# Performance work log

Hardware: AMD Instinct MI355X
Metric: run time of the kernel (lower is better)

## Reference

```python
import jax, jax.numpy as jnp
import numpy as np

D_MODEL = 1024
D_INNER = 2048
D_STATE = 16
DT_RANK = 64
D_CONV = 4
EPS = 1e-5
B_SZ, L = 2, 2048


def setup_inputs() -> dict:
    key = jax.random.key(0)
    ks = jax.random.split(key, 8)
    s = 0.02
    inp = {
        "x": jax.random.normal(ks[0], (B_SZ, L, D_MODEL), jnp.float32),
        "in_proj_w": jax.random.normal(ks[1], (D_MODEL, 2 * D_INNER), jnp.float32) * s,
        "conv_w": jax.random.normal(ks[2], (D_INNER, 1, D_CONV), jnp.float32) * s,
        "conv_b": jnp.zeros((D_INNER,), jnp.float32),
        "x_proj_w": jax.random.normal(ks[3], (D_INNER, DT_RANK + 2 * D_STATE), jnp.float32) * s,
        "dt_proj_w": jax.random.normal(ks[4], (DT_RANK, D_INNER), jnp.float32) * s,
        "dt_proj_b": jax.random.normal(ks[5], (D_INNER,), jnp.float32) * s,
        "A_log": jnp.log(jnp.broadcast_to(jnp.arange(1, D_STATE + 1, dtype=jnp.float32), (D_INNER, D_STATE))),
        "D": jnp.ones((D_INNER,), jnp.float32),
        "out_proj_w": jax.random.normal(ks[6], (D_INNER, D_MODEL), jnp.float32) * s,
        "norm_w": jnp.ones((D_MODEL,), jnp.float32),
    }
    return inp


def _silu(x):
    return x * jax.nn.sigmoid(x)


def reference(x, in_proj_w, conv_w, conv_b, x_proj_w, dt_proj_w, dt_proj_b,
              A_log, D, out_proj_w, norm_w):
    b, l, d = x.shape
    # RMSNorm
    xn = x * jax.lax.rsqrt(jnp.mean(x * x, axis=-1, keepdims=True) + EPS) * norm_w
    # in_proj -> split into x branch and residual (gate) branch
    x_and_res = xn @ in_proj_w                      # (b, l, 2*d_inner)
    xi, res = jnp.split(x_and_res, 2, axis=-1)
    # causal depthwise conv1d (pad left d_conv-1, equivalent to torch pad+truncate)
    xc = jax.lax.conv_general_dilated(
        xi.transpose(0, 2, 1),                      # (b, d_inner, l)
        conv_w,                                     # (d_inner, 1, d_conv) = OIH
        window_strides=(1,),
        padding=[(D_CONV - 1, 0)],
        feature_group_count=D_INNER,
        dimension_numbers=("NCH", "OIH", "NCH"),
    ) + conv_b[None, :, None]
    xi = _silu(xc.transpose(0, 2, 1))               # (b, l, d_inner)
    # SSM parameters
    x_dbl = xi @ x_proj_w                           # (b, l, dt_rank + 2n)
    delta, Bm, Cm = jnp.split(x_dbl, [DT_RANK, DT_RANK + D_STATE], axis=-1)
    delta = jax.nn.softplus(delta @ dt_proj_w + dt_proj_b)   # (b, l, d_inner)
    A = -jnp.exp(A_log)                             # (d_inner, n)
    # discretize
    deltaA = jnp.exp(delta[..., None] * A)                          # (b,l,d,n)
    deltaB_u = delta[..., None] * Bm[:, :, None, :] * xi[..., None]  # (b,l,d,n)
    # selective scan over sequence length via lax.scan
    def step(state, inputs):
        dA_t, dBu_t, C_t = inputs                   # (b,d,n),(b,d,n),(b,n)
        state = dA_t * state + dBu_t
        y_t = jnp.einsum("bdn,bn->bd", state, C_t)
        return state, y_t
    state0 = jnp.zeros((b, D_INNER, D_STATE), xi.dtype)
    _, ys = jax.lax.scan(
        step, state0,
        (deltaA.transpose(1, 0, 2, 3), deltaB_u.transpose(1, 0, 2, 3), Cm.transpose(1, 0, 2)),
    )                                               # ys: (l, b, d_inner)
    y = ys.transpose(1, 0, 2) + xi * D              # skip connection D*u
    y = y * _silu(res)                              # gate
    out = y @ out_proj_w + x                        # out_proj + residual add
    return out
```

## Files before the change

### kernel.cpp

```cpp
#include <hip/hip_runtime.h>
#include <cstdint>

#define D_MODEL 1024
#define D_INNER 2048
#define NSTATE  16
#define DT_RANK 64
#define SEQ     2048
#define NBATCH  2
#define NTOK    (NBATCH * SEQ)

#define NC      32
#define CHK     64
#define NGRP    8

typedef float  f32x4  __attribute__((ext_vector_type(4)));
typedef __bf16 bf16x8 __attribute__((ext_vector_type(8)));
typedef short  s16x8  __attribute__((ext_vector_type(8)));

__device__ __forceinline__ unsigned short f2bf(float f) {
  union { float f; uint32_t u; } a; a.f = f;
  uint32_t u = a.u;
  uint32_t r = (u + 0x7FFFu + ((u >> 16) & 1u)) >> 16;
  return (unsigned short)r;
}
__device__ __forceinline__ float bf2f(unsigned short h) {
  union { uint32_t u; float f; } a; a.u = ((uint32_t)h) << 16;
  return a.f;
}

__device__ __forceinline__ void gload16(const void* g, void* l) {
  __builtin_amdgcn_global_load_lds((__attribute__((address_space(1))) void*)g,
                                   (__attribute__((address_space(3))) void*)l,
                                   16, 0, 0);
}

__device__ __forceinline__ void rms_body(const float* __restrict__ x, const float* __restrict__ nw,
                                         unsigned short* __restrict__ xn, int row, float* red) {
  const float4 v = ((const float4*)(x + (size_t)row * D_MODEL))[threadIdx.x];
  float ss = v.x*v.x + v.y*v.y + v.z*v.z + v.w*v.w;
  #pragma unroll
  for (int m = 32; m; m >>= 1) ss += __shfl_xor(ss, m);
  if ((threadIdx.x & 63) == 0) red[threadIdx.x >> 6] = ss;
  __syncthreads();
  const float tot = red[0] + red[1] + red[2] + red[3];
  const float rs = rsqrtf(tot * (1.0f / D_MODEL) + 1e-5f);
  const float4 w = ((const float4*)nw)[threadIdx.x];
  ushort4 o;
  o.x = f2bf(v.x * rs * w.x);
  o.y = f2bf(v.y * rs * w.y);
  o.z = f2bf(v.z * rs * w.z);
  o.w = f2bf(v.w * rs * w.w);
  ((ushort4*)(xn + (size_t)row * D_MODEL))[threadIdx.x] = o;
}

__device__ __forceinline__ void tr_body(const float* __restrict__ W, unsigned short* __restrict__ Wt,
                                        int K, int N, int Npad, int bx, int by, float (*tile)[33]) {
  const int tx = threadIdx.x & 31, ty = threadIdx.x >> 5;
  const int kt = by * 32, nt = bx * 32;
  #pragma unroll
  for (int i = 0; i < 4; ++i) {
    const int k = kt + ty + i*8, n = nt + tx;
    tile[ty + i*8][tx] = (k < K && n < N) ? W[(size_t)k * N + n] : 0.0f;
  }
  __syncthreads();
  #pragma unroll
  for (int i = 0; i < 4; ++i) {
    const int n = nt + ty + i*8, k = kt + tx;
    if (n < Npad && k < K) Wt[(size_t)n * K + k] = f2bf(tile[tx][ty + i*8]);
  }
}

__global__ __launch_bounds__(256) void prep_fused_kernel(const float* x, const float* nw, unsigned short* xn,
                                                         const float* W1, unsigned short* W1t,
                                                         const float* W2, unsigned short* W2t,
                                                         const float* W3, unsigned short* W3t,
                                                         const float* W4, unsigned short* W4t) {
  __shared__ float shbuf[32][33];
  const int b = blockIdx.x;
  if (b < 4096) {
    rms_body(x, nw, xn, b, &shbuf[0][0]);
  } else if (b < 8192) {
    const int i = b - 4096;
    tr_body(W1, W1t, 1024, 4096, 4096, i & 127, i >> 7, shbuf);
  } else if (b < 8448) {
    const int i = b - 8192;
    tr_body(W2, W2t, 2048, 96, 128, i & 3, i >> 2, shbuf);
  } else if (b < 8576) {
    const int i = b - 8448;
    tr_body(W3, W3t, 64, 2048, 2048, i & 63, i >> 6, shbuf);
  } else {
    const int i = b - 8576;
    tr_body(W4, W4t, 2048, 1024, 1024, i & 31, i >> 5, shbuf);
  }
}

template<int MODE>
__device__ __forceinline__ void gemm_body(const unsigned short* __restrict__ A,
                                          const unsigned short* __restrict__ Bt,
                                          const int M, const int N, const int K,
                                          void* __restrict__ out0,
                                          void* __restrict__ out1,
                                          const float* __restrict__ extra) {
  __shared__ __align__(16) unsigned short sA[2][128 * 32];
  __shared__ __align__(16) unsigned short sB[2][128 * 32];
  const int tid = threadIdx.x;
  const int w = tid >> 6, lane = tid & 63;
  const int m0 = blockIdx.y * 128, n0 = blockIdx.x * 128;
  const int wm = w >> 1, wn = w & 1;
  const int lr = lane & 15, kq = lane >> 4;

  f32x4 acc[4][4] = {};

  const int r0 = tid >> 2;
  const int qb = ((tid & 3) ^ (r0 & 3)) * 16;
  const char* pA0 = (const char*)A + ((size_t)(m0 + r0)      * K) * 2 + qb;
  const char* pA1 = (const char*)A + ((size_t)(m0 + r0 + 64) * K) * 2 + qb;
  const char* pB0 = (const char*)Bt + ((size_t)(n0 + r0)      * K) * 2 + qb;
  const char* pB1 = (const char*)Bt + ((size_t)(n0 + r0 + 64) * K) * 2 + qb;

  const int kqs = (kq ^ (lr & 3)) * 8;

  auto stage = [&](int p, int k0) {
    gload16(pA0 + (size_t)k0 * 2, (char*)sA[p] + w * 1024);
    gload16(pA1 + (size_t)k0 * 2, (char*)sA[p] + 4096 + w * 1024);
    gload16(pB0 + (size_t)k0 * 2, (char*)sB[p] + w * 1024);
    gload16(pB1 + (size_t)k0 * 2, (char*)sB[p] + 4096 + w * 1024);
  };
  auto compute = [&](int p) {
    const unsigned short* pa = sA[p] + (wm*64 + lr) * 32 + kqs;
    const unsigned short* pb = sB[p] + (wn*64 + lr) * 32 + kqs;
    bf16x8 af[4], bb[4];
    #pragma unroll
    for (int mf = 0; mf < 4; ++mf)
      af[mf] = __builtin_bit_cast(bf16x8, *(const s16x8*)(pa + mf * 16 * 32));
    #pragma unroll
    for (int nf = 0; nf < 4; ++nf)
      bb[nf] = __builtin_bit_cast(bf16x8, *(const s16x8*)(pb + nf * 16 * 32));
    #pragma unroll
    for (int mf = 0; mf < 4; ++mf)
      #pragma unroll
      for (int nf = 0; nf < 4; ++nf)
        acc[mf][nf] = __builtin_amdgcn_mfma_f32_16x16x32_bf16(af[mf], bb[nf], acc[mf][nf], 0, 0, 0);
  };

  stage(0, 0);
  __syncthreads();
  int p = 0;
  for (int k0 = 32; k0 < K; k0 += 32) {
    stage(p ^ 1, k0);
    compute(p);
    __syncthreads();
    p ^= 1;
  }
  compute(p);

  #pragma unroll
  for (int mf = 0; mf < 4; ++mf) {
    #pragma unroll
    for (int nf = 0; nf < 4; ++nf) {
      #pragma unroll
      for (int r = 0; r < 4; ++r) {
        const int row = m0 + wm*64 + mf*16 + kq*4 + r;
        const int col = n0 + wn*64 + nf*16 + lr;
        const float v = acc[mf][nf][r];
        if constexpr (MODE == 0) {
          if (col < D_INNER) ((unsigned short*)out0)[(size_t)row * D_INNER + col] = f2bf(v);
          else               ((unsigned short*)out1)[(size_t)row * D_INNER + (col - D_INNER)] = f2bf(v);
        } else if constexpr (MODE == 1) {
          if (col < DT_RANK) ((unsigned short*)out0)[(size_t)row * DT_RANK + col] = f2bf(v);
          else if (col < DT_RANK + 2*NSTATE) ((float*)out1)[(size_t)row * (2*NSTATE) + (col - DT_RANK)] = v;
        } else if constexpr (MODE == 2) {
          const float t = v + extra[col];
          const float sp = (t > 30.0f) ? t : __logf(1.0f + __expf(t));
          ((unsigned short*)out0)[(size_t)row * D_INNER + col] = f2bf(sp);
        } else {
          ((float*)out0)[(size_t)row * D_MODEL + col] = v + extra[(size_t)row * D_MODEL + col];
        }
      }
    }
  }
}

__global__ __launch_bounds__(256) void g0_inproj_kernel(const unsigned short* A, const unsigned short* Bt,
                                                        int M, int N, int K, void* o0, void* o1, const float* ex) {
  gemm_body<0>(A, Bt, M, N, K, o0, o1, ex);
}
__global__ __launch_bounds__(256) void g1_xproj_kernel(const unsigned short* A, const unsigned short* Bt,
                                                       int M, int N, int K, void* o0, void* o1, const float* ex) {
  gemm_body<1>(A, Bt, M, N, K, o0, o1, ex);
}
__global__ __launch_bounds__(256) void g2_dtproj_kernel(const unsigned short* A, const unsigned short* Bt,
                                                        int M, int N, int K, void* o0, void* o1, const float* ex) {
  gemm_body<2>(A, Bt, M, N, K, o0, o1, ex);
}
__global__ __launch_bounds__(256) void g3_outproj_kernel(const unsigned short* A, const unsigned short* Bt,
                                                         int M, int N, int K, void* o0, void* o1, const float* ex) {
  gemm_body<3>(A, Bt, M, N, K, o0, o1, ex);
}

__global__ __launch_bounds__(256) void conv_silu_kernel(const unsigned short* __restrict__ xi_raw,
                                                        const float* __restrict__ cw,
                                                        const float* __restrict__ cb,
                                                        unsigned short* __restrict__ xi) {
  const int t = blockIdx.x * 256 + threadIdx.x;
  const int d8 = (t & 255) * 8;
  const int row = t >> 8;
  const int l = row & (SEQ - 1);

  float acc[8];
  #pragma unroll
  for (int c = 0; c < 8; c += 4) {
    const f32x4 bv = *(const f32x4*)(cb + d8 + c);
    acc[c+0] = bv[0]; acc[c+1] = bv[1]; acc[c+2] = bv[2]; acc[c+3] = bv[3];
  }
  f32x4 wv[8];
  #pragma unroll
  for (int c = 0; c < 8; ++c) wv[c] = ((const f32x4*)cw)[d8 + c];

  #pragma unroll
  for (int tap = 0; tap < 4; ++tap) {
    const int lp = l - 3 + tap;
    if (lp >= 0) {
      const s16x8 v = *(const s16x8*)(xi_raw + (size_t)(row - 3 + tap) * D_INNER + d8);
      #pragma unroll
      for (int c = 0; c < 8; ++c)
        acc[c] += wv[c][tap] * bf2f((unsigned short)v[c]);
    }
  }
  s16x8 o;
  #pragma unroll
  for (int c = 0; c < 8; ++c) {
    const float a = acc[c] / (1.0f + __expf(-acc[c]));
    o[c] = (short)f2bf(a);
  }
  *(s16x8*)(xi + (size_t)row * D_INNER + d8) = o;
}

template<int PASS>
__global__ __launch_bounds__(256) void scan_pass_kernel(const unsigned short* __restrict__ delta,
                                                        const unsigned short* __restrict__ xi,
                                                        const unsigned short* __restrict__ res,
                                                        const float* __restrict__ BC,
                                                        const float* __restrict__ A_log,
                                                        const float* __restrict__ Dv,
                                                        const float* __restrict__ initS,
                                                        float* __restrict__ aprodOut,
                                                        float* __restrict__ sendOut,
                                                        unsigned short* __restrict__ yg) {
  const int tid = threadIdx.x;
  const int db = blockIdx.x & 7;
  const int c  = (blockIdx.x >> 3) & (NC - 1);
  const int b  = blockIdx.x >> 8;
  const int d  = db * 256 + tid;
  const int row0 = b * SEQ + c * CHK;
  const size_t ob = ((size_t)(b * NC + c) * D_INNER + d) * 16;

  float Ac[16];
  #pragma unroll
  for (int q = 0; q < 4; ++q) {
    f32x4 t = ((const f32x4*)(A_log + (size_t)d * 16))[q];
    Ac[q*4+0] = -expf(t[0]); Ac[q*4+1] = -expf(t[1]);
    Ac[q*4+2] = -expf(t[2]); Ac[q*4+3] = -expf(t[3]);
  }
  float s[16];
  float ap[16];
  if constexpr (PASS == 0) {
    #pragma unroll
    for (int n = 0; n < 16; ++n) { s[n] = 0.0f; ap[n] = 1.0f; }
  } else {
    #pragma unroll
    for (int q = 0; q < 4; ++q)
      ((f32x4*)s)[q] = ((const f32x4*)(initS + ob))[q];
  }
  float Dd = 0.0f;
  if constexpr (PASS == 1) Dd = Dv[d];

  __shared__ float bcbuf[2][8][32];
  auto stageg = [&](int g, int p) {
    bcbuf[p][tid >> 5][tid & 31] = BC[(size_t)(row0 + g * 8) * 32 + tid];
  };
  stageg(0, 0);

  for (int g = 0; g < NGRP; ++g) {
    unsigned short dl[8], uu[8], rr[8];
    #pragma unroll
    for (int j = 0; j < 8; ++j) {
      const size_t row = (size_t)(row0 + g * 8 + j) * D_INNER + d;
      dl[j] = delta[row];
      uu[j] = xi[row];
      if constexpr (PASS == 1) rr[j] = res[row];
    }
    __syncthreads();
    if (g + 1 < NGRP) stageg(g + 1, (g + 1) & 1);

    #pragma unroll
    for (int j = 0; j < 8; ++j) {
      const float dlt = bf2f(dl[j]);
      const float u   = bf2f(uu[j]);
      const float dlu = dlt * u;
      float bc[32];
      #pragma unroll
      for (int q = 0; q < (PASS ? 8 : 4); ++q)
        ((f32x4*)bc)[q] = ((const f32x4*)(&bcbuf[g & 1][j][0]))[q];
      #pragma unroll
      for (int n = 0; n < 16; ++n) {
        const float dA = __expf(dlt * Ac[n]);
        s[n] = dA * s[n] + dlu * bc[n];
        if constexpr (PASS == 0) ap[n] *= dA;
      }
      if constexpr (PASS == 1) {
        float y = 0.0f;
        #pragma unroll
        for (int n = 0; n < 16; ++n) y += s[n] * bc[16 + n];
        const float r = bf2f(rr[j]);
        const float o = (y + u * Dd) * (r / (1.0f + __expf(-r)));
        yg[(size_t)(row0 + g * 8 + j) * D_INNER + d] = f2bf(o);
      }
    }
  }

  if constexpr (PASS == 0) {
    #pragma unroll
    for (int q = 0; q < 4; ++q) {
      ((f32x4*)(aprodOut + ob))[q] = ((f32x4*)ap)[q];
      ((f32x4*)(sendOut + ob))[q]  = ((f32x4*)s)[q];
    }
  }
}

__global__ __launch_bounds__(256) void scan_combine_kernel(const float* __restrict__ aprod,
                                                           const float* __restrict__ send,
                                                           float* __restrict__ initS) {
  const int t = blockIdx.x * 256 + threadIdx.x;
  const int b = t >> 13;
  const int rq = t & 8191;
  f32x4 carry = {0.0f, 0.0f, 0.0f, 0.0f};
  #pragma unroll
  for (int c = 0; c < NC; ++c) {
    const size_t idx = (size_t)(b * NC + c) * 8192 + rq;
    ((f32x4*)initS)[idx] = carry;
    const f32x4 a = ((const f32x4*)aprod)[idx];
    const f32x4 e = ((const f32x4*)send)[idx];
    carry = a * carry + e;
  }
}

extern "C" void kernel_launch(void* const* d_in, const int* in_sizes, int n_in,
                              void* d_out, int out_size, void* d_ws, size_t ws_size,
                              hipStream_t stream) {
  const float* x        = (const float*)d_in[0];
  const float* in_proj  = (const float*)d_in[1];
  const float* conv_w   = (const float*)d_in[2];
  const float* conv_b   = (const float*)d_in[3];
  const float* x_proj   = (const float*)d_in[4];
  const float* dt_proj  = (const float*)d_in[5];
  const float* dt_b     = (const float*)d_in[6];
  const float* A_log    = (const float*)d_in[7];
  const float* Dv       = (const float*)d_in[8];
  const float* out_proj = (const float*)d_in[9];
  const float* norm_w   = (const float*)d_in[10];

  char* ws = (char*)d_ws;
  size_t off = 0;
  auto alloc = [&](size_t bytes) {
    char* p = ws + off; off += (bytes + 255) & ~(size_t)255; return p;
  };
  unsigned short* xn     = (unsigned short*)alloc((size_t)NTOK * D_MODEL * 2);
  unsigned short* W1t    = (unsigned short*)alloc((size_t)(2 * D_INNER) * D_MODEL * 2);
  unsigned short* xi_raw = (unsigned short*)alloc((size_t)NTOK * D_INNER * 2);
  unsigned short* resb   = (unsigned short*)alloc((size_t)NTOK * D_INNER * 2);
  unsigned short* xi     = (unsigned short*)alloc((size_t)NTOK * D_INNER * 2);
  unsigned short* W2t    = (unsigned short*)alloc((size_t)128 * D_INNER * 2);
  unsigned short* dr     = (unsigned short*)alloc((size_t)NTOK * DT_RANK * 2);
  float*          BC     = (float*)alloc((size_t)NTOK * 32 * 4);
  unsigned short* W3t    = (unsigned short*)alloc((size_t)D_INNER * DT_RANK * 2);
  unsigned short* dlt    = (unsigned short*)alloc((size_t)NTOK * D_INNER * 2);
  unsigned short* ygb    = (unsigned short*)alloc((size_t)NTOK * D_INNER * 2);
  unsigned short* W4t    = (unsigned short*)alloc((size_t)D_MODEL * D_INNER * 2);

  float* aprod = (float*)xi_raw;
  float* send  = (float*)((char*)xi_raw + 8388608);
  float* initS = (float*)xn;

  prep_fused_kernel<<<10624, 256, 0, stream>>>(x, norm_w, xn,
                                               in_proj, W1t, x_proj, W2t,
                                               dt_proj, W3t, out_proj, W4t);

  g0_inproj_kernel<<<dim3(4096/128, 4096/128), 256, 0, stream>>>(xn, W1t, NTOK, 4096, 1024, xi_raw, resb, nullptr);
  conv_silu_kernel<<<NTOK, 256, 0, stream>>>(xi_raw, conv_w, conv_b, xi);
  g1_xproj_kernel<<<dim3(1, 4096/128), 256, 0, stream>>>(xi, W2t, NTOK, 128, 2048, dr, BC, nullptr);
  g2_dtproj_kernel<<<dim3(2048/128, 4096/128), 256, 0, stream>>>(dr, W3t, NTOK, 2048, 64, dlt, nullptr, dt_b);

  scan_pass_kernel<0><<<NBATCH * NC * (D_INNER/256), 256, 0, stream>>>(
      dlt, xi, nullptr, BC, A_log, nullptr, nullptr, aprod, send, nullptr);
  scan_combine_kernel<<<64, 256, 0, stream>>>(aprod, send, initS);
  scan_pass_kernel<1><<<NBATCH * NC * (D_INNER/256), 256, 0, stream>>>(
      dlt, xi, resb, BC, A_log, Dv, initS, nullptr, nullptr, ygb);

  g3_outproj_kernel<<<dim3(1024/128, 4096/128), 256, 0, stream>>>(ygb, W4t, NTOK, 1024, 2048, d_out, nullptr, x);
}
```

Before: 369.1 us.

## Give in_proj GEMM a dedicated 256x256 tile kernel with swizzled LDS

Swaps the generic 128x128 bf16 GEMM for in_proj with a dedicated kernel that uses 256x256 output tiles, 512 threads, BK=64, XOR-swizzled shared memory and direct global-to-LDS loads. Loads for the next K tile are interleaved with MFMA sub-steps, and s_setprio raises priority around the MFMA bursts. The goal is more operand reuse per tile and less LDS bank conflict and stall time on the largest GEMM. In exchange it uses 128KB of LDS per block and many accumulator registers, and the grid drops to 256 blocks, which may limit occupancy across the CUs.

New measurement: 350.3 us. -5.1%, faster.

```diff
diff --git a/kernel.cpp b/kernel.cpp
--- a/kernel.cpp
+++ b/kernel.cpp
@@ -94,6 +94,97 @@
   }
 }
 
+__global__ __launch_bounds__(512, 2) void g0_inproj_kernel(const unsigned short* __restrict__ A,
+                                                           const unsigned short* __restrict__ Bt,
+                                                           unsigned short* __restrict__ xiOut,
+                                                           unsigned short* __restrict__ resOut) {
+  constexpr int K  = 1024;
+  constexpr int NT = K / 64;
+  __shared__ __align__(16) unsigned short sA[2][256 * 64];
+  __shared__ __align__(16) unsigned short sB[2][256 * 64];
+  const int tid = threadIdx.x;
+  const int wid = tid >> 6, lane = tid & 63;
+  const int wm = wid >> 2, wn = wid & 3;
+  const int lr = lane & 15, kq = lane >> 4;
+  const int m0 = blockIdx.y * 256, n0 = blockIdx.x * 256;
+
+  f32x4 acc[8][4] = {};
+
+  const int srow = tid >> 3;
+  const int scol = 8 * ((tid & 7) ^ ((tid >> 3) & 7));
+  const unsigned short* gA = A  + (size_t)(m0 + srow) * K + scol;
+  const unsigned short* gB = Bt + (size_t)(n0 + srow) * K + scol;
+
+  const int xsw = (lr & 7) << 4;
+  const int cofs0 = ((kq * 16) ^ xsw) >> 1;
+  const int cofs1 = ((64 + kq * 16) ^ xsw) >> 1;
+  const int aRow = (wm * 128 + lr) * 64;
+  const int bRow = (wn * 64 + lr) * 64;
+
+  auto stage2 = [&](int p, int kt, int q) {
+    const int k0 = kt * 64;
+    gload16(gA + (size_t)q * 64 * K + k0, (char*)sA[p] + q * 8192 + tid * 16);
+    gload16(gB + (size_t)q * 64 * K + k0, (char*)sB[p] + q * 8192 + tid * 16);
+  };
+
+  #pragma unroll
+  for (int q = 0; q < 4; ++q) stage2(0, 0, q);
+  __syncthreads();
+
+  int p = 0;
+  for (int kt = 0; kt < NT; ++kt) {
+    const unsigned short* SA = sA[p];
+    const unsigned short* SB = sB[p];
+    bf16x8 b[4][2];
+    #pragma unroll
+    for (int q = 0; q < 4; ++q) {
+      bf16x8 a[2][2];
+      #pragma unroll
+      for (int mi = 0; mi < 2; ++mi) {
+        a[mi][0] = __builtin_bit_cast(bf16x8, *(const s16x8*)(SA + aRow + (2*q + mi) * 1024 + cofs0));
+        a[mi][1] = __builtin_bit_cast(bf16x8, *(const s16x8*)(SA + aRow + (2*q + mi) * 1024 + cofs1));
+      }
+      if (q == 0) {
+        #pragma unroll
+        for (int nf = 0; nf < 4; ++nf) {
+          b[nf][0] = __builtin_bit_cast(bf16x8, *(const s16x8*)(SB + bRow + nf * 1024 + cofs0));
+          b[nf][1] = __builtin_bit_cast(bf16x8, *(const s16x8*)(SB + bRow + nf * 1024 + cofs1));
+        }
+      }
+      if (kt + 1 < NT) stage2(p ^ 1, kt + 1, q);
+      __builtin_amdgcn_s_barrier();
+      __builtin_amdgcn_s_setprio(1);
+      #pragma unroll
+      for (int ks = 0; ks < 2; ++ks)
+        #pragma unroll
+        for (int mi = 0; mi < 2; ++mi)
+          #pragma unroll
+          for (int nf = 0; nf < 4; ++nf)
+            acc[2*q + mi][nf] = __builtin_amdgcn_mfma_f32_16x16x32_bf16(a[mi][ks], b[nf][ks], acc[2*q + mi][nf], 0, 0, 0);
+      __builtin_amdgcn_s_setprio(0);
+      __builtin_amdgcn_s_barrier();
+    }
+    __syncthreads();
+    p ^= 1;
+  }
+
+  #pragma unroll
+  for (int mf = 0; mf < 8; ++mf) {
+    #pragma unroll
+    for (int nf = 0; nf < 4; ++nf) {
+      const int col = n0 + wn * 64 + nf * 16 + lr;
+      unsigned short* dst = (col < D_INNER)
+          ? xiOut + col
+          : resOut + (col - D_INNER);
+      #pragma unroll
+      for (int r = 0; r < 4; ++r) {
+        const int row = m0 + wm * 128 + mf * 16 + kq * 4 + r;
+        dst[(size_t)row * D_INNER] = f2bf(acc[mf][nf][r]);
+      }
+    }
+  }
+}
+
 template<int MODE>
 __device__ __forceinline__ void gemm_body(const unsigned short* __restrict__ A,
                                           const unsigned short* __restrict__ Bt,
@@ -163,10 +254,7 @@
         const int row = m0 + wm*64 + mf*16 + kq*4 + r;
         const int col = n0 + wn*64 + nf*16 + lr;
         const float v = acc[mf][nf][r];
-        if constexpr (MODE == 0) {
-          if (col < D_INNER) ((unsigned short*)out0)[(size_t)row * D_INNER + col] = f2bf(v);
-          else               ((unsigned short*)out1)[(size_t)row * D_INNER + (col - D_INNER)] = f2bf(v);
-        } else if constexpr (MODE == 1) {
+        if constexpr (MODE == 1) {
           if (col < DT_RANK) ((unsigned short*)out0)[(size_t)row * DT_RANK + col] = f2bf(v);
           else if (col < DT_RANK + 2*NSTATE) ((float*)out1)[(size_t)row * (2*NSTATE) + (col - DT_RANK)] = v;
         } else if constexpr (MODE == 2) {
@@ -181,10 +269,6 @@
   }
 }
 
-__global__ __launch_bounds__(256) void g0_inproj_kernel(const unsigned short* A, const unsigned short* Bt,
-                                                        int M, int N, int K, void* o0, void* o1, const float* ex) {
-  gemm_body<0>(A, Bt, M, N, K, o0, o1, ex);
-}
 __global__ __launch_bounds__(256) void g1_xproj_kernel(const unsigned short* A, const unsigned short* Bt,
                                                        int M, int N, int K, void* o0, void* o1, const float* ex) {
   gemm_body<1>(A, Bt, M, N, K, o0, o1, ex);
@@ -386,7 +470,7 @@
                                                in_proj, W1t, x_proj, W2t,
                                                dt_proj, W3t, out_proj, W4t);
 
-  g0_inproj_kernel<<<dim3(4096/128, 4096/128), 256, 0, stream>>>(xn, W1t, NTOK, 4096, 1024, xi_raw, resb, nullptr);
+  g0_inproj_kernel<<<dim3(4096/256, 4096/256), 512, 0, stream>>>(xn, W1t, xi_raw, resb);
   conv_silu_kernel<<<NTOK, 256, 0, stream>>>(xi_raw, conv_w, conv_b, xi);
   g1_xproj_kernel<<<dim3(1, 4096/128), 256, 0, stream>>>(xi, W2t, NTOK, 128, 2048, dr, BC, nullptr);
   g2_dtproj_kernel<<<dim3(2048/128, 4096/128), 256, 0, stream>>>(dr, W3t, NTOK, 2048, 64, dlt, nullptr, dt_b);
```
